# Kernel optimization log

Hardware: AMD Instinct MI355X
Metric: run time of the kernel (lower is better)

## Reference

```python
import jax, jax.numpy as jnp
import numpy as np

LATENT = 1024
HIDDEN = 4096
ENC = 1024
HEADS = 16
HEAD_DIM = LATENT // HEADS
B, SQ, SK = 4, 1024, 1024
EPS = 1e-5


def _linear(x, w, b):
    # torch nn.Linear: y = x @ w.T + b, w shape (out, in)
    return jnp.einsum('bsi,oi->bso', x, w) + b


def _mha(Q, K, wq, bq, wk, bk, wv, bv, wo, bo):
    Bq, Sq, _ = Q.shape
    Sk = K.shape[1]
    Qp = _linear(Q, wq, bq).reshape(Bq, Sq, HEADS, HEAD_DIM)
    Kp = _linear(K, wk, bk).reshape(Bq, Sk, HEADS, HEAD_DIM)
    Vp = _linear(K, wv, bv).reshape(Bq, Sk, HEADS, HEAD_DIM)
    # NOTE: original scales by 1/sqrt(latent_size), not 1/sqrt(head_dim)
    E = jnp.einsum('bqhd,bkhd->bhqk', Qp, Kp) / np.sqrt(LATENT).astype(np.float32)
    A = jax.nn.softmax(E, axis=-1)
    O = jnp.einsum('bhqk,bkhd->bqhd', A, Vp).reshape(Bq, Sq, LATENT)
    return _linear(O, wo, bo)


def _ln(x, g, b):
    mu = jnp.mean(x, axis=-1, keepdims=True)
    var = jnp.mean((x - mu) ** 2, axis=-1, keepdims=True)
    return (x - mu) * jax.lax.rsqrt(var + EPS) * g + b


def setup_inputs() -> dict:
    key = jax.random.key(0)
    ks = jax.random.split(key, 32)
    s = 0.02
    d = {
        'Q': jax.random.normal(ks[0], (B, SQ, LATENT), jnp.float32),
        'K': jax.random.normal(ks[1], (B, SK, ENC), jnp.float32),
        'a1_wq': jax.random.normal(ks[2], (LATENT, LATENT)) * s,
        'a1_bq': jnp.zeros((LATENT,)),
        'a1_wk': jax.random.normal(ks[3], (LATENT, LATENT)) * s,
        'a1_bk': jnp.zeros((LATENT,)),
        'a1_wv': jax.random.normal(ks[4], (LATENT, LATENT)) * s,
        'a1_bv': jnp.zeros((LATENT,)),
        'a1_wo': jax.random.normal(ks[5], (LATENT, LATENT)) * s,
        'a1_bo': jnp.zeros((LATENT,)),
        'a2_wq': jax.random.normal(ks[6], (LATENT, LATENT)) * s,
        'a2_bq': jnp.zeros((LATENT,)),
        'a2_wk': jax.random.normal(ks[7], (LATENT, ENC)) * s,
        'a2_bk': jnp.zeros((LATENT,)),
        'a2_wv': jax.random.normal(ks[8], (LATENT, ENC)) * s,
        'a2_bv': jnp.zeros((LATENT,)),
        'a2_wo': jax.random.normal(ks[9], (LATENT, LATENT)) * s,
        'a2_bo': jnp.zeros((LATENT,)),
        'fc_w1': jax.random.normal(ks[10], (HIDDEN, LATENT)) * s,
        'fc_b1': jnp.zeros((HIDDEN,)),
        'fc_w2': jax.random.normal(ks[11], (LATENT, HIDDEN)) * s,
        'fc_b2': jnp.zeros((LATENT,)),
        'ln0_g': jnp.ones((LATENT,)), 'ln0_b': jnp.zeros((LATENT,)),
        'ln1_g': jnp.ones((LATENT,)), 'ln1_b': jnp.zeros((LATENT,)),
        'ln2_g': jnp.ones((LATENT,)), 'ln2_b': jnp.zeros((LATENT,)),
    }
    return d


def reference(Q, K, a1_wq, a1_bq, a1_wk, a1_bk, a1_wv, a1_bv, a1_wo, a1_bo,
              a2_wq, a2_bq, a2_wk, a2_bk, a2_wv, a2_bv, a2_wo, a2_bo,
              fc_w1, fc_b1, fc_w2, fc_b2,
              ln0_g, ln0_b, ln1_g, ln1_b, ln2_g, ln2_b):
    # self-attention block
    A1 = _mha(Q, Q, a1_wq, a1_bq, a1_wk, a1_bk, a1_wv, a1_bv, a1_wo, a1_bo)
    X = _ln(Q + A1, ln0_g, ln0_b)
    # cross-attention block
    A2 = _mha(X, K, a2_wq, a2_bq, a2_wk, a2_bk, a2_wv, a2_bv, a2_wo, a2_bo)
    X = _ln(X + A2, ln1_g, ln1_b)
    # FFN: Linear -> ReLU -> Linear
    FC = _linear(jax.nn.relu(_linear(X, fc_w1, fc_b1)), fc_w2, fc_b2)
    X = _ln(X + FC, ln2_g, ln2_b)
    return X
```

## Files before the change

### kernel.cpp

```cpp
#include <hip/hip_runtime.h>
#include <hip/hip_bf16.h>
#include <math.h>

#define LATENT 1024
#define HIDDEN 4096
#define HEADS 16
#define HEAD_DIM 64
#define BATCH 4
#define SQL 1024
#define SKL 1024

typedef __bf16 bf16;
typedef __attribute__((ext_vector_type(4))) __bf16 bf16x4;
typedef __attribute__((ext_vector_type(8))) __bf16 bf16x8;
typedef __attribute__((ext_vector_type(4))) float f32x4;

#define MFMA16 __builtin_amdgcn_mfma_f32_16x16x32_bf16

__device__ __forceinline__ void async_ld16(const bf16* g, bf16* l) {
    __builtin_amdgcn_global_load_lds(
        (const __attribute__((address_space(1))) unsigned int*)g,
        (__attribute__((address_space(3))) unsigned int*)l,
        16, 0, 0);
}

__global__ void detect_dtype(const void* g, int* flag) {
    if (threadIdx.x == 0) *flag = (*(const float*)g == 1.0f) ? 1 : 0;
}

struct CanonArgs {
    const void* src[28];
    bf16* dst[28];
    int n[28];
};

__global__ __launch_bounds__(256) void canonicalize(CanonArgs a, const int* flagp) {
    const int buf = blockIdx.y;
    const int n = a.n[buf];
    const int i0 = (blockIdx.x * 256 + threadIdx.x) * 8;
    if (i0 >= n) return;
    bf16* dst = a.dst[buf];
    if (*flagp) {
        const float* s = (const float*)a.src[buf];
        float4 u0 = *(const float4*)(s + i0);
        float4 u1 = *(const float4*)(s + i0 + 4);
        bf16x8 o;
        o[0] = (bf16)u0.x; o[1] = (bf16)u0.y; o[2] = (bf16)u0.z; o[3] = (bf16)u0.w;
        o[4] = (bf16)u1.x; o[5] = (bf16)u1.y; o[6] = (bf16)u1.z; o[7] = (bf16)u1.w;
        *(bf16x8*)(dst + i0) = o;
    } else {
        *(bf16x8*)(dst + i0) = *(const bf16x8*)((const bf16*)a.src[buf] + i0);
    }
}

template<int BN, bool RELU>
__global__ __launch_bounds__(256, 2)
void gemm2(const bf16* __restrict__ A, const bf16* __restrict__ W,
           const bf16* __restrict__ bias,
           bf16* __restrict__ out0, bf16* __restrict__ out1, bf16* __restrict__ outT,
           int M, int N, int K, int nNormal, int ostride) {
    constexpr int WAVES_N = BN / 64;
    constexpr int WAVES_M = 4 / WAVES_N;
    constexpr int WM = 128 / WAVES_M;
    constexpr int MI = WM / 16;
    constexpr int BROWS = BN / 4;
    __shared__ alignas(16) bf16 smem[(128 + BN) * 64];
    bf16* lA = smem;
    bf16* lB = smem + 128 * 64;
    const int tid  = threadIdx.x;
    const int w    = tid >> 6;
    const int lane = tid & 63;
    const int quad = lane >> 4;
    const int l16  = lane & 15;
    const int bm = blockIdx.y * 128;
    const int bn = blockIdx.x * BN;
    const int wr = w / WAVES_N, wc = w % WAVES_N;

    f32x4 acc[MI][4] = {};

    const int srow = lane >> 3;
    const int schk = (lane & 7) * 8;
    const bf16* Abase = A + (long)(bm + w * 32 + srow) * K + schk;
    const bf16* Wbase = W + (long)(bn + w * BROWS + srow) * K + schk;
    bf16* lAw = lA + (w * 32 + srow) * 64 + schk;
    bf16* lBw = lB + (w * BROWS + srow) * 64 + schk;

    for (int k0 = 0; k0 < K; k0 += 64) {
        __syncthreads();
#pragma unroll
        for (int i = 0; i < 4; ++i)
            async_ld16(Abase + k0 + (long)(i * 8) * K, lAw + i * 8 * 64);
#pragma unroll
        for (int i = 0; i < BROWS / 8; ++i)
            async_ld16(Wbase + k0 + (long)(i * 8) * K, lBw + i * 8 * 64);
        __syncthreads();
#pragma unroll
        for (int ks = 0; ks < 2; ++ks) {
            bf16x8 af[MI], bfv[4];
#pragma unroll
            for (int i = 0; i < MI; ++i)
                af[i] = *(const bf16x8*)&lA[(wr * WM + i * 16 + l16) * 64 + ks * 32 + quad * 8];
#pragma unroll
            for (int j = 0; j < 4; ++j)
                bfv[j] = *(const bf16x8*)&lB[(wc * 64 + j * 16 + l16) * 64 + ks * 32 + quad * 8];
#pragma unroll
            for (int i = 0; i < MI; ++i)
#pragma unroll
                for (int j = 0; j < 4; ++j)
                    acc[i][j] = MFMA16(af[i], bfv[j], acc[i][j], 0, 0, 0);
        }
    }

    float bvv[4];
#pragma unroll
    for (int j = 0; j < 4; ++j) bvv[j] = (float)bias[bn + wc * 64 + j * 16 + l16];

    if (bn < nNormal) {
        bf16* base = out0;
        int colb = bn;
        if (out1 && colb >= 1024) { base = out1; colb -= 1024; }
#pragma unroll
        for (int i = 0; i < MI; ++i) {
#pragma unroll
            for (int r = 0; r < 4; ++r) {
                const int row = bm + wr * WM + i * 16 + quad * 4 + r;
#pragma unroll
                for (int j = 0; j < 4; ++j) {
                    float v = acc[i][j][r] + bvv[j];
                    if (RELU) v = fmaxf(v, 0.f);
                    base[(long)row * ostride + colb + wc * 64 + j * 16 + l16] = (bf16)v;
                }
            }
        }
    } else {
        const int n0v = bn - nNormal;
        __syncthreads();
#pragma unroll
        for (int p = 0; p < 2; ++p) {
            if (p) __syncthreads();
            if (wc == p) {
#pragma unroll
                for (int i = 0; i < MI; ++i)
#pragma unroll
                    for (int j = 0; j < 4; ++j) {
                        const int colL = j * 16 + l16;
                        const int rowL = wr * WM + i * 16 + quad * 4;
                        bf16x4 pk;
#pragma unroll
                        for (int r = 0; r < 4; ++r) pk[r] = (bf16)(acc[i][j][r] + bvv[j]);
                        *(bf16x4*)&smem[colL * 136 + rowL] = pk;
                    }
            }
            __syncthreads();
#pragma unroll
            for (int k = 0; k < 8; ++k) {
                const int c = tid + k * 256;
                const int rL = c >> 5, ch = c & 31;
                *(bf16x4*)&outT[(long)(n0v + p * 64 + rL) * M + bm + ch * 4] =
                    *(const bf16x4*)&smem[rL * 136 + ch * 4];
            }
        }
    }
}

__global__ __launch_bounds__(256, 3)
void attn2(const bf16* __restrict__ Qp, const bf16* __restrict__ Kp,
           const bf16* __restrict__ Vt, bf16* __restrict__ O) {
    __shared__ alignas(16) bf16 lQ[64 * 64];
    __shared__ alignas(16) bf16 lK[2][64 * 64];
    __shared__ alignas(16) bf16 lV[2][64 * 64];
    __shared__ alignas(16) bf16 lP[4][16 * 64];
    const int tid  = threadIdx.x;
    const int w    = tid >> 6;
    const int lane = tid & 63;
    const int quad = lane >> 4;
    const int l16  = lane & 15;
    const int b  = blockIdx.z;
    const int h  = blockIdx.y;
    const int q0 = blockIdx.x * 64;

#pragma unroll
    for (int s = 0; s < 2; ++s) {
        const int c = w * 128 + s * 64 + lane;
        const int row = c >> 3, ch = (c & 7) * 8;
        async_ld16(Qp + (long)(b * SQL + q0 + row) * LATENT + h * 64 + ch, lQ + c * 8);
    }
#define STAGE_KV(buf, kt)                                                        \
    {                                                                            \
        _Pragma("unroll")                                                        \
        for (int s = 0; s < 2; ++s) {                                            \
            const int c = w * 128 + s * 64 + lane;                               \
            const int row = c >> 3, ch = (c & 7) * 8;                            \
            async_ld16(Kp + (long)(b * SKL + (kt) * 64 + row) * LATENT + h * 64 + ch, \
                       &lK[buf][c * 8]);                                         \
            async_ld16(Vt + (long)(h * 64 + row) * (BATCH * SKL) + b * SKL + (kt) * 64 + ch, \
                       &lV[buf][c * 8]);                                         \
        }                                                                        \
    }
    STAGE_KV(0, 0);
    __syncthreads();

    bf16x8 aq[2];
    aq[0] = *(const bf16x8*)&lQ[(w * 16 + l16) * 64 + quad * 8];
    aq[1] = *(const bf16x8*)&lQ[(w * 16 + l16) * 64 + 32 + quad * 8];

    f32x4 o_acc[4] = {};
    float lsum[4] = {0.f, 0.f, 0.f, 0.f};

    for (int kt = 0; kt < SKL / 64; ++kt) {
        const int cur = kt & 1;
        if (kt < SKL / 64 - 1) STAGE_KV(cur ^ 1, kt + 1);

        f32x4 s4[4] = {};
#pragma unroll
        for (int ks = 0; ks < 2; ++ks)
#pragma unroll
            for (int j = 0; j < 4; ++j) {
                bf16x8 bk = *(const bf16x8*)&lK[cur][(j * 16 + l16) * 64 + ks * 32 + quad * 8];
                s4[j] = MFMA16(aq[ks], bk, s4[j], 0, 0, 0);
            }

#pragma unroll
        for (int r = 0; r < 4; ++r)
#pragma unroll
            for (int j = 0; j < 4; ++j) {
                const float p = __expf(s4[j][r] * 0.03125f);
                lsum[r] += p;
                lP[w][(quad * 4 + r) * 64 + j * 16 + l16] = (bf16)p;
            }
        __asm__ volatile("s_waitcnt lgkmcnt(0)" ::: "memory");

#pragma unroll
        for (int ks = 0; ks < 2; ++ks) {
            bf16x8 ap = *(const bf16x8*)&lP[w][l16 * 64 + ks * 32 + quad * 8];
#pragma unroll
            for (int j = 0; j < 4; ++j) {
                bf16x8 bv = *(const bf16x8*)&lV[cur][(j * 16 + l16) * 64 + ks * 32 + quad * 8];
                o_acc[j] = MFMA16(ap, bv, o_acc[j], 0, 0, 0);
            }
        }
        __syncthreads();
    }

#pragma unroll
    for (int r = 0; r < 4; ++r) {
#pragma unroll
        for (int off = 1; off <= 8; off <<= 1)
            lsum[r] += __shfl_xor(lsum[r], off, 64);
    }
#pragma unroll
    for (int r = 0; r < 4; ++r) {
        const float inv = 1.f / lsum[r];
        const int row = q0 + w * 16 + quad * 4 + r;
#pragma unroll
        for (int j = 0; j < 4; ++j)
            O[(long)(b * SQL + row) * LATENT + h * 64 + j * 16 + l16] = (bf16)(o_acc[j][r] * inv);
    }
#undef STAGE_KV
}

template<bool F32OUT>
__global__ __launch_bounds__(256)
void ln_kernel(const bf16* __restrict__ res, const bf16* __restrict__ y,
               const bf16* __restrict__ g, const bf16* __restrict__ bta,
               bf16* __restrict__ outres, void* __restrict__ outb) {
    const int row = blockIdx.x;
    const int tid = threadIdx.x;
    const long base = (long)row * LATENT;
    const int c = tid * 4;
    bf16x4 rv = *(const bf16x4*)&res[base + c];
    bf16x4 yv = *(const bf16x4*)&y[base + c];
    float x[4];
    float s1 = 0.f, s2 = 0.f;
#pragma unroll
    for (int i = 0; i < 4; ++i) {
        float v = (float)rv[i] + (float)yv[i];
        x[i] = v; s1 += v; s2 += v * v;
    }
#pragma unroll
    for (int off = 32; off >= 1; off >>= 1) {
        s1 += __shfl_xor(s1, off, 64);
        s2 += __shfl_xor(s2, off, 64);
    }
    __shared__ float ps1[4], ps2[4];
    const int w = tid >> 6, lane = tid & 63;
    if (lane == 0) { ps1[w] = s1; ps2[w] = s2; }
    __syncthreads();
    s1 = ps1[0] + ps1[1] + ps1[2] + ps1[3];
    s2 = ps2[0] + ps2[1] + ps2[2] + ps2[3];
    const float mu = s1 * (1.f / LATENT);
    const float var = s2 * (1.f / LATENT) - mu * mu;
    const float rstd = rsqrtf(var + 1e-5f);
    bf16x4 gv = *(const bf16x4*)&g[c];
    bf16x4 bv = *(const bf16x4*)&bta[c];
    float o[4];
#pragma unroll
    for (int i = 0; i < 4; ++i)
        o[i] = (x[i] - mu) * rstd * (float)gv[i] + (float)bv[i];
    if (F32OUT) {
        float4 f; f.x = o[0]; f.y = o[1]; f.z = o[2]; f.w = o[3];
        *(float4*)&((float*)outb)[base + c] = f;
    } else {
        bf16x4 bo;
#pragma unroll
        for (int i = 0; i < 4; ++i) bo[i] = (bf16)o[i];
        *(bf16x4*)&((bf16*)outb)[base + c] = bo;
        if (outres) *(bf16x4*)&outres[base + c] = bo;
    }
}

extern "C" void kernel_launch(void* const* d_in, const int* in_sizes, int n_in,
                              void* d_out, int out_size, void* d_ws, size_t ws_size,
                              hipStream_t stream) {
    char* ws = (char*)d_ws;

    static const int order[28] = {2, 4, 6, 3, 5, 7, 12, 14, 13, 15,
                                  0, 1, 8, 9, 10, 11, 16, 17, 18, 19,
                                  20, 21, 22, 23, 24, 25, 26, 27};
    size_t coff[28];
    size_t cur = 256;
    for (int k = 0; k < 28; ++k) {
        const int i = order[k];
        coff[i] = cur;
        cur += (((size_t)in_sizes[i] * 2) + 255) & ~(size_t)255;
    }
    const size_t canon_end = (cur + 255) & ~(size_t)255;
    const size_t MB8 = 8ull << 20;
    const size_t need = canon_end + 7 * MB8;
    const bool full = ws_size >= need;

    const bf16* cv[28];
    if (full) {
        int* flag = (int*)ws;
        detect_dtype<<<dim3(1), dim3(64), 0, stream>>>(d_in[22], flag);
        CanonArgs ca;
        for (int i = 0; i < 28; ++i) {
            ca.src[i] = d_in[i];
            ca.dst[i] = (bf16*)(ws + coff[i]);
            ca.n[i]   = in_sizes[i];
            cv[i]     = (const bf16*)(ws + coff[i]);
        }
        canonicalize<<<dim3(2048, 28), dim3(256), 0, stream>>>(ca, flag);
    } else {
        for (int i = 0; i < 28; ++i) cv[i] = (const bf16*)d_in[i];
    }

    const size_t base = full ? canon_end : 0;
    bf16* Xres = (bf16*)(ws + base);
    bf16* Yf   = (bf16*)(ws + base + 1 * MB8);
    bf16* Xb   = (bf16*)(ws + base + 2 * MB8);
    bf16* Qp   = (bf16*)(ws + base + 3 * MB8);
    bf16* Kp   = (bf16*)(ws + base + 4 * MB8);
    bf16* Vt   = (bf16*)(ws + base + 5 * MB8);
    bf16* AttO = (bf16*)(ws + base + 6 * MB8);
    bf16* H    = Qp;

    const bf16 *Qc = cv[0], *Kc = cv[1];
    const int M = BATCH * SQL;
    dim3 blk(256);
    dim3 ga(SQL / 64, HEADS, BATCH);

    gemm2<128, false><<<dim3(3072 / 128, M / 128), blk, 0, stream>>>(
        Qc, cv[2], cv[3], Qp, Kp, Vt, M, 3072, LATENT, 2048, 1024);
    attn2<<<ga, blk, 0, stream>>>(Qp, Kp, Vt, AttO);
    gemm2<64, false><<<dim3(1024 / 64, M / 128), blk, 0, stream>>>(
        AttO, cv[8], cv[9], Yf, nullptr, nullptr, M, 1024, LATENT, 1024, 1024);
    ln_kernel<false><<<dim3(M), blk, 0, stream>>>(Qc, Yf, cv[22], cv[23], Xres, Xb);

    gemm2<64, false><<<dim3(1024 / 64, M / 128), blk, 0, stream>>>(
        Xb, cv[10], cv[11], Qp, nullptr, nullptr, M, 1024, LATENT, 1024, 1024);
    gemm2<128, false><<<dim3(2048 / 128, M / 128), blk, 0, stream>>>(
        Kc, cv[12], cv[13], Kp, nullptr, Vt, M, 2048, LATENT, 1024, 1024);
    attn2<<<ga, blk, 0, stream>>>(Qp, Kp, Vt, AttO);
    gemm2<64, false><<<dim3(1024 / 64, M / 128), blk, 0, stream>>>(
        AttO, cv[16], cv[17], Yf, nullptr, nullptr, M, 1024, LATENT, 1024, 1024);
    ln_kernel<false><<<dim3(M), blk, 0, stream>>>(Xres, Yf, cv[24], cv[25], Xres, Xb);

    gemm2<128, true><<<dim3(4096 / 128, M / 128), blk, 0, stream>>>(
        Xb, cv[18], cv[19], H, nullptr, nullptr, M, HIDDEN, LATENT, 4096, 4096);
    gemm2<64, false><<<dim3(1024 / 64, M / 128), blk, 0, stream>>>(
        H, cv[20], cv[21], Yf, nullptr, nullptr, M, 1024, HIDDEN, 1024, 1024);
    ln_kernel<true><<<dim3(M), blk, 0, stream>>>(Xres, Yf, cv[26], cv[27], nullptr, d_out);
}
```

Before: 548.6 us.

## Double-buffer GEMM LDS tiles with K=32 steps and bank-friendly swizzled layout

After: 632.2 us. 15.2% more time.

```diff
diff --git a/kernel.cpp b/kernel.cpp
--- a/kernel.cpp
+++ b/kernel.cpp
@@ -63,10 +63,10 @@
     constexpr int WAVES_M = 4 / WAVES_N;
     constexpr int WM = 128 / WAVES_M;
     constexpr int MI = WM / 16;
-    constexpr int BROWS = BN / 4;
-    __shared__ alignas(16) bf16 smem[(128 + BN) * 64];
-    bf16* lA = smem;
-    bf16* lB = smem + 128 * 64;
+    constexpr int ASZ = 128 * 32;
+    constexpr int BSZ = BN * 32;
+    constexpr int NBS = (BN * 4) / 256;
+    __shared__ alignas(16) bf16 smem[2 * (ASZ + BSZ)];
     const int tid  = threadIdx.x;
     const int w    = tid >> 6;
     const int lane = tid & 63;
@@ -78,38 +78,70 @@
 
     f32x4 acc[MI][4] = {};
 
-    const int srow = lane >> 3;
-    const int schk = (lane & 7) * 8;
-    const bf16* Abase = A + (long)(bm + w * 32 + srow) * K + schk;
-    const bf16* Wbase = W + (long)(bn + w * BROWS + srow) * K + schk;
-    bf16* lAw = lA + (w * 32 + srow) * 64 + schk;
-    bf16* lBw = lB + (w * BROWS + srow) * 64 + schk;
-
-    for (int k0 = 0; k0 < K; k0 += 64) {
+    const bf16* gAs[2]; int lAoff[2];
+#pragma unroll
+    for (int i = 0; i < 2; ++i) {
+        const int s   = w * 128 + i * 64 + lane;
+        const int row = ((s >> 5) << 3) + (s & 7);
+        const int ch  = ((s >> 3) & 3) << 3;
+        gAs[i]   = A + (long)(bm + row) * K + ch;
+        lAoff[i] = s * 8;
+    }
+    const bf16* gBs[NBS]; int lBoff[NBS];
+#pragma unroll
+    for (int i = 0; i < NBS; ++i) {
+        const int s   = w * (64 * NBS) + i * 64 + lane;
+        const int row = ((s >> 5) << 3) + (s & 7);
+        const int ch  = ((s >> 3) & 3) << 3;
+        gBs[i]   = W + (long)(bn + row) * K + ch;
+        lBoff[i] = s * 8;
+    }
+
+    int offA[MI], offB[4];
+#pragma unroll
+    for (int i = 0; i < MI; ++i) {
+        const int row = wr * WM + i * 16 + l16;
+        offA[i] = ((row >> 3) << 8) + ((row & 7) << 3) + (quad << 6);
+    }
+#pragma unroll
+    for (int j = 0; j < 4; ++j) {
+        const int row = wc * 64 + j * 16 + l16;
+        offB[j] = ((row >> 3) << 8) + ((row & 7) << 3) + (quad << 6);
+    }
+
+#define STAGE_G(bufp, kk)                                                      \
+    {                                                                          \
+        bf16* lAc_ = smem + (bufp) * (ASZ + BSZ);                              \
+        bf16* lBc_ = lAc_ + ASZ;                                               \
+        _Pragma("unroll")                                                      \
+        for (int i_ = 0; i_ < 2; ++i_)                                         \
+            async_ld16(gAs[i_] + (kk), lAc_ + lAoff[i_]);                      \
+        _Pragma("unroll")                                                      \
+        for (int i_ = 0; i_ < NBS; ++i_)                                       \
+            async_ld16(gBs[i_] + (kk), lBc_ + lBoff[i_]);                      \
+    }
+
+    STAGE_G(0, 0);
+    __syncthreads();
+    const int NK = K >> 5;
+    for (int kt = 0; kt < NK; ++kt) {
+        const int cur = kt & 1;
+        if (kt + 1 < NK) STAGE_G(cur ^ 1, (kt + 1) << 5);
+        const bf16* lAc = smem + cur * (ASZ + BSZ);
+        const bf16* lBc = lAc + ASZ;
+        bf16x8 af[MI], bfv[4];
+#pragma unroll
+        for (int i = 0; i < MI; ++i) af[i] = *(const bf16x8*)&lAc[offA[i]];
+#pragma unroll
+        for (int j = 0; j < 4; ++j) bfv[j] = *(const bf16x8*)&lBc[offB[j]];
+#pragma unroll
+        for (int i = 0; i < MI; ++i)
+#pragma unroll
+            for (int j = 0; j < 4; ++j)
+                acc[i][j] = MFMA16(af[i], bfv[j], acc[i][j], 0, 0, 0);
         __syncthreads();
-#pragma unroll
-        for (int i = 0; i < 4; ++i)
-            async_ld16(Abase + k0 + (long)(i * 8) * K, lAw + i * 8 * 64);
-#pragma unroll
-        for (int i = 0; i < BROWS / 8; ++i)
-            async_ld16(Wbase + k0 + (long)(i * 8) * K, lBw + i * 8 * 64);
-        __syncthreads();
-#pragma unroll
-        for (int ks = 0; ks < 2; ++ks) {
-            bf16x8 af[MI], bfv[4];
-#pragma unroll
-            for (int i = 0; i < MI; ++i)
-                af[i] = *(const bf16x8*)&lA[(wr * WM + i * 16 + l16) * 64 + ks * 32 + quad * 8];
-#pragma unroll
-            for (int j = 0; j < 4; ++j)
-                bfv[j] = *(const bf16x8*)&lB[(wc * 64 + j * 16 + l16) * 64 + ks * 32 + quad * 8];
-#pragma unroll
-            for (int i = 0; i < MI; ++i)
-#pragma unroll
-                for (int j = 0; j < 4; ++j)
-                    acc[i][j] = MFMA16(af[i], bfv[j], acc[i][j], 0, 0, 0);
-        }
-    }
+    }
+#undef STAGE_G
 
     float bvv[4];
 #pragma unroll
```

## Swizzle GEMM LDS layout, remap workgroups for L2 locality, unify 128x128 tiles

Applied to the files above, without the earlier changes.

New measurement: 660.6 us. 20.4% more time.

```diff
diff --git a/kernel.cpp b/kernel.cpp
--- a/kernel.cpp
+++ b/kernel.cpp
@@ -53,58 +53,64 @@
     }
 }
 
-template<int BN, bool RELU>
+template<bool RELU>
 __global__ __launch_bounds__(256, 2)
-void gemm2(const bf16* __restrict__ A, const bf16* __restrict__ W,
+void gemm3(const bf16* __restrict__ A, const bf16* __restrict__ W,
            const bf16* __restrict__ bias,
            bf16* __restrict__ out0, bf16* __restrict__ out1, bf16* __restrict__ outT,
            int M, int N, int K, int nNormal, int ostride) {
-    constexpr int WAVES_N = BN / 64;
-    constexpr int WAVES_M = 4 / WAVES_N;
-    constexpr int WM = 128 / WAVES_M;
-    constexpr int MI = WM / 16;
-    constexpr int BROWS = BN / 4;
-    __shared__ alignas(16) bf16 smem[(128 + BN) * 64];
-    bf16* lA = smem;
-    bf16* lB = smem + 128 * 64;
+    constexpr int ASZ = 128 * 64;
+    __shared__ alignas(16) bf16 smem[2 * ASZ];
+    bf16* lB = smem + ASZ;
     const int tid  = threadIdx.x;
     const int w    = tid >> 6;
     const int lane = tid & 63;
     const int quad = lane >> 4;
     const int l16  = lane & 15;
-    const int bm = blockIdx.y * 128;
-    const int bn = blockIdx.x * BN;
-    const int wr = w / WAVES_N, wc = w % WAVES_N;
-
-    f32x4 acc[MI][4] = {};
-
-    const int srow = lane >> 3;
-    const int schk = (lane & 7) * 8;
-    const bf16* Abase = A + (long)(bm + w * 32 + srow) * K + schk;
-    const bf16* Wbase = W + (long)(bn + w * BROWS + srow) * K + schk;
-    bf16* lAw = lA + (w * 32 + srow) * 64 + schk;
-    bf16* lBw = lB + (w * BROWS + srow) * 64 + schk;
+    const int nx  = gridDim.x;
+    const int nwg = nx * gridDim.y;
+    int bid = blockIdx.y * nx + blockIdx.x;
+    bid = (bid & 7) * (nwg >> 3) + (bid >> 3);
+    const int bm = (bid / nx) * 128;
+    const int bn = (bid % nx) * 128;
+    const int wr = w >> 1, wc = w & 1;
+
+    f32x4 acc[4][4] = {};
+
+    const int srow = ((tid >> 6) << 3) | (tid & 7);
+    const int sch  = ((tid >> 3) & 7) << 3;
+    const bf16* gA = A + (long)(bm + srow) * K + sch;
+    const bf16* gW = W + (long)(bn + srow) * K + sch;
+    const long r32 = 32 * (long)K;
+    bf16* lA0 = smem + tid * 8;
+    bf16* lB0 = lB + tid * 8;
+
+    int offA[4], offB[4];
+#pragma unroll
+    for (int i = 0; i < 4; ++i) {
+        const int ra = wr * 64 + i * 16 + l16;
+        offA[i] = ((ra >> 3) << 9) + ((ra & 7) << 3) + (quad << 6);
+        const int rb = wc * 64 + i * 16 + l16;
+        offB[i] = ((rb >> 3) << 9) + ((rb & 7) << 3) + (quad << 6);
+    }
 
     for (int k0 = 0; k0 < K; k0 += 64) {
         __syncthreads();
 #pragma unroll
-        for (int i = 0; i < 4; ++i)
-            async_ld16(Abase + k0 + (long)(i * 8) * K, lAw + i * 8 * 64);
-#pragma unroll
-        for (int i = 0; i < BROWS / 8; ++i)
-            async_ld16(Wbase + k0 + (long)(i * 8) * K, lBw + i * 8 * 64);
+        for (int i = 0; i < 4; ++i) {
+            async_ld16(gA + k0 + i * r32, lA0 + i * 2048);
+            async_ld16(gW + k0 + i * r32, lB0 + i * 2048);
+        }
         __syncthreads();
 #pragma unroll
         for (int ks = 0; ks < 2; ++ks) {
-            bf16x8 af[MI], bfv[4];
-#pragma unroll
-            for (int i = 0; i < MI; ++i)
-                af[i] = *(const bf16x8*)&lA[(wr * WM + i * 16 + l16) * 64 + ks * 32 + quad * 8];
-#pragma unroll
-            for (int j = 0; j < 4; ++j)
-                bfv[j] = *(const bf16x8*)&lB[(wc * 64 + j * 16 + l16) * 64 + ks * 32 + quad * 8];
-#pragma unroll
-            for (int i = 0; i < MI; ++i)
+            bf16x8 af[4], bfv[4];
+#pragma unroll
+            for (int i = 0; i < 4; ++i) af[i]  = *(const bf16x8*)&smem[offA[i] + ks * 256];
+#pragma unroll
+            for (int j = 0; j < 4; ++j) bfv[j] = *(const bf16x8*)&lB[offB[j] + ks * 256];
+#pragma unroll
+            for (int i = 0; i < 4; ++i)
 #pragma unroll
                 for (int j = 0; j < 4; ++j)
                     acc[i][j] = MFMA16(af[i], bfv[j], acc[i][j], 0, 0, 0);
@@ -120,10 +126,10 @@
         int colb = bn;
         if (out1 && colb >= 1024) { base = out1; colb -= 1024; }
 #pragma unroll
-        for (int i = 0; i < MI; ++i) {
+        for (int i = 0; i < 4; ++i) {
 #pragma unroll
             for (int r = 0; r < 4; ++r) {
-                const int row = bm + wr * WM + i * 16 + quad * 4 + r;
+                const int row = bm + wr * 64 + i * 16 + quad * 4 + r;
 #pragma unroll
                 for (int j = 0; j < 4; ++j) {
                     float v = acc[i][j][r] + bvv[j];
@@ -140,11 +146,11 @@
             if (p) __syncthreads();
             if (wc == p) {
 #pragma unroll
-                for (int i = 0; i < MI; ++i)
+                for (int i = 0; i < 4; ++i)
 #pragma unroll
                     for (int j = 0; j < 4; ++j) {
                         const int colL = j * 16 + l16;
-                        const int rowL = wr * WM + i * 16 + quad * 4;
+                        const int rowL = wr * 64 + i * 16 + quad * 4;
                         bf16x4 pk;
 #pragma unroll
                         for (int r = 0; r < 4; ++r) pk[r] = (bf16)(acc[i][j][r] + bvv[j]);
@@ -360,25 +366,25 @@
     dim3 blk(256);
     dim3 ga(SQL / 64, HEADS, BATCH);
 
-    gemm2<128, false><<<dim3(3072 / 128, M / 128), blk, 0, stream>>>(
+    gemm3<false><<<dim3(3072 / 128, M / 128), blk, 0, stream>>>(
         Qc, cv[2], cv[3], Qp, Kp, Vt, M, 3072, LATENT, 2048, 1024);
     attn2<<<ga, blk, 0, stream>>>(Qp, Kp, Vt, AttO);
-    gemm2<64, false><<<dim3(1024 / 64, M / 128), blk, 0, stream>>>(
+    gemm3<false><<<dim3(1024 / 128, M / 128), blk, 0, stream>>>(
         AttO, cv[8], cv[9], Yf, nullptr, nullptr, M, 1024, LATENT, 1024, 1024);
     ln_kernel<false><<<dim3(M), blk, 0, stream>>>(Qc, Yf, cv[22], cv[23], Xres, Xb);
 
-    gemm2<64, false><<<dim3(1024 / 64, M / 128), blk, 0, stream>>>(
+    gemm3<false><<<dim3(1024 / 128, M / 128), blk, 0, stream>>>(
         Xb, cv[10], cv[11], Qp, nullptr, nullptr, M, 1024, LATENT, 1024, 1024);
-    gemm2<128, false><<<dim3(2048 / 128, M / 128), blk, 0, stream>>>(
+    gemm3<false><<<dim3(2048 / 128, M / 128), blk, 0, stream>>>(
         Kc, cv[12], cv[13], Kp, nullptr, Vt, M, 2048, LATENT, 1024, 1024);
     attn2<<<ga, blk, 0, stream>>>(Qp, Kp, Vt, AttO);
-    gemm2<64, false><<<dim3(1024 / 64, M / 128), blk, 0, stream>>>(
+    gemm3<false><<<dim3(1024 / 128, M / 128), blk, 0, stream>>>(
         AttO, cv[16], cv[17], Yf, nullptr, nullptr, M, 1024, LATENT, 1024, 1024);
     ln_kernel<false><<<dim3(M), blk, 0, stream>>>(Xres, Yf, cv[24], cv[25], Xres, Xb);
 
-    gemm2<128, true><<<dim3(4096 / 128, M / 128), blk, 0, stream>>>(
+    gemm3<true><<<dim3(4096 / 128, M / 128), blk, 0, stream>>>(
         Xb, cv[18], cv[19], H, nullptr, nullptr, M, HIDDEN, LATENT, 4096, 4096);
-    gemm2<64, false><<<dim3(1024 / 64, M / 128), blk, 0, stream>>>(
+    gemm3<false><<<dim3(1024 / 128, M / 128), blk, 0, stream>>>(
         H, cv[20], cv[21], Yf, nullptr, nullptr, M, 1024, HIDDEN, 1024, 1024);
     ln_kernel<true><<<dim3(M), blk, 0, stream>>>(Xres, Yf, cv[26], cv[27], nullptr, d_out);
 }
```

## Double-buffer GEMM LDS tiles to overlap async global loads with MFMA

Applied to the files above, without the earlier changes.

Result: faster. 520.5 us (-5.1%).

```diff
diff --git a/kernel.cpp b/kernel.cpp
--- a/kernel.cpp
+++ b/kernel.cpp
@@ -64,9 +64,8 @@
     constexpr int WM = 128 / WAVES_M;
     constexpr int MI = WM / 16;
     constexpr int BROWS = BN / 4;
-    __shared__ alignas(16) bf16 smem[(128 + BN) * 64];
-    bf16* lA = smem;
-    bf16* lB = smem + 128 * 64;
+    constexpr int BUFSZ = (128 + BN) * 64;
+    __shared__ alignas(16) bf16 smem[2 * BUFSZ];
     const int tid  = threadIdx.x;
     const int w    = tid >> 6;
     const int lane = tid & 63;
@@ -82,18 +81,30 @@
     const int schk = (lane & 7) * 8;
     const bf16* Abase = A + (long)(bm + w * 32 + srow) * K + schk;
     const bf16* Wbase = W + (long)(bn + w * BROWS + srow) * K + schk;
-    bf16* lAw = lA + (w * 32 + srow) * 64 + schk;
-    bf16* lBw = lB + (w * BROWS + srow) * 64 + schk;
-
+    const int lAoff = (w * 32 + srow) * 64 + schk;
+    const int lBoff = 128 * 64 + (w * BROWS + srow) * 64 + schk;
+
+#define STAGE_G(bufp, kk)                                                      \
+    {                                                                          \
+        bf16* bb_ = smem + (bufp) * BUFSZ;                                     \
+        _Pragma("unroll")                                                      \
+        for (int i_ = 0; i_ < 4; ++i_)                                         \
+            async_ld16(Abase + (kk) + (long)(i_ * 8) * K, bb_ + lAoff + i_ * 8 * 64); \
+        _Pragma("unroll")                                                      \
+        for (int i_ = 0; i_ < BROWS / 8; ++i_)                                 \
+            async_ld16(Wbase + (kk) + (long)(i_ * 8) * K, bb_ + lBoff + i_ * 8 * 64); \
+    }
+
+    STAGE_G(0, 0);
+    __asm__ volatile("s_waitcnt vmcnt(0)" ::: "memory");
+    __builtin_amdgcn_s_barrier();
+    __builtin_amdgcn_sched_barrier(0);
+
+    int cur = 0;
     for (int k0 = 0; k0 < K; k0 += 64) {
-        __syncthreads();
-#pragma unroll
-        for (int i = 0; i < 4; ++i)
-            async_ld16(Abase + k0 + (long)(i * 8) * K, lAw + i * 8 * 64);
-#pragma unroll
-        for (int i = 0; i < BROWS / 8; ++i)
-            async_ld16(Wbase + k0 + (long)(i * 8) * K, lBw + i * 8 * 64);
-        __syncthreads();
+        if (k0 + 64 < K) STAGE_G(cur ^ 1, k0 + 64);
+        const bf16* lA = smem + cur * BUFSZ;
+        const bf16* lB = lA + 128 * 64;
 #pragma unroll
         for (int ks = 0; ks < 2; ++ks) {
             bf16x8 af[MI], bfv[4];
@@ -109,7 +120,12 @@
                 for (int j = 0; j < 4; ++j)
                     acc[i][j] = MFMA16(af[i], bfv[j], acc[i][j], 0, 0, 0);
         }
-    }
+        __asm__ volatile("s_waitcnt vmcnt(0)" ::: "memory");
+        __builtin_amdgcn_s_barrier();
+        __builtin_amdgcn_sched_barrier(0);
+        cur ^= 1;
+    }
+#undef STAGE_G
 
     float bvv[4];
 #pragma unroll
```
